# Optimization experiments

Hardware: AMD Instinct MI355X
Metric: run time of the kernel (lower is better)

The kernel has to match this reference:

```python
import jax, jax.numpy as jnp
import numpy as np

REF_POINTS = 32
WINDOW_HOURS = 48.0


def setup_inputs() -> dict:
    key = jax.random.key(0)
    k1, k2, k3 = jax.random.split(key, 3)
    B, T, F = 32, 512, 128
    x_hat = jax.random.normal(k1, (B, T, F), dtype=jnp.float32)
    mask = jax.random.randint(k2, (B, T, F), 0, 2).astype(jnp.float32)
    # per-step deltas in seconds (~0-600s) so cumulative time spans the 48h window
    tau = jax.random.uniform(k3, (B, T), dtype=jnp.float32) * 600.0
    log_kernel = jnp.zeros((F,), dtype=jnp.float32)
    return {"x_hat": x_hat, "mask": mask, "tau": tau, "log_kernel": log_kernel}


def reference(x_hat, mask, tau, log_kernel):
    # x_hat, mask: (B,T,F); tau: (B,T); log_kernel: (F,)
    kappa = jax.nn.softplus(log_kernel)                       # (F,)
    t_hours = jnp.cumsum(tau, axis=1) / 3600.0                # (B,T)
    ref_t = jnp.linspace(0.0, WINDOW_HOURS, REF_POINTS, dtype=x_hat.dtype)  # (R,)
    dist2 = (t_hours[:, :, None] - ref_t[None, None, :]) ** 2  # (B,T,R)
    d2k = dist2[..., None] * kappa                             # (B,T,R,F)
    m = mask[:, :, None, :]                                    # (B,T,1,F) -> broadcast over R
    w_lp = jnp.exp(-d2k) * m                                   # (B,T,R,F)
    w_hp = jnp.exp(-10.0 * d2k) * m                            # (B,T,R,F)
    x4 = x_hat[:, :, None, :]                                  # (B,T,1,F)
    lam = jnp.sum(w_lp, axis=1)                                # (B,R,F)
    sigma = jnp.sum(w_lp * x4, axis=1) / jnp.maximum(lam, 1.0)
    gamma = jnp.sum(w_hp * x4, axis=1) / jnp.maximum(jnp.sum(w_hp, axis=1), 1.0)
    return sigma, lam, gamma
```

## Files before the change

kernel.cpp:

```cpp
#include <hip/hip_runtime.h>
#include <math.h>
#include <type_traits>

constexpr int B_ = 32, T_ = 512, F_ = 128, R_ = 32;
constexpr int OUT_STRIDE = B_ * R_ * F_;

__device__ __forceinline__ float exp2_fast(float v) { return __builtin_amdgcn_exp2f(v); }

__launch_bounds__(256, 4)
__global__ void gauss_all(const float* __restrict__ xh, const float* __restrict__ mk,
                          const float* __restrict__ tau, const float* __restrict__ logk,
                          float* __restrict__ out) {
    const int lin = blockIdx.x;
    const int xcd = lin & 7, idx = lin >> 3;
    const int g = idx >> 5;
    const int r = (idx + g * 8) & 31;
    const int b = xcd + 8 * g;

    const int tid = threadIdx.x, lane = tid & 63, w = tid >> 6;
    __shared__ float th_s[T_];
    __shared__ float red[8][64];
    for (int i = tid; i < 512; i += 256) ((float*)red)[i] = 0.f;

    const float* tb = tau + b * T_;
    float v[8]; float s = 0.f;
#pragma unroll
    for (int k = 0; k < 8; ++k) { s += tb[lane * 8 + k]; v[k] = s; }
    float x = s;
#pragma unroll
    for (int d = 1; d < 64; d <<= 1) { float y = __shfl_up(x, d, 64); if (lane >= d) x += y; }
    const float excl = x - s;
#pragma unroll
    for (int k = 0; k < 8; ++k) v[k] = (excl + v[k]) * (1.f / 3600.f);
    if (w == 0) {
#pragma unroll
        for (int k = 0; k < 8; ++k) th_s[lane * 8 + k] = v[k];
    }

    const int f0 = 2 * lane;
    const float L2E = 1.4426950408889634f;
    const float lkx = logk[f0], lky = logk[f0 + 1];
    const float spx = fmaxf(lkx, 0.f) + log1pf(expf(-fabsf(lkx)));
    const float spy = fmaxf(lky, 0.f) + log1pf(expf(-fabsf(lky)));
    float mn = fminf(spx, spy), mx = fmaxf(spx, spy);
#pragma unroll
    for (int d = 1; d < 64; d <<= 1) {
        mn = fminf(mn, __shfl_xor(mn, d, 64));
        mx = fmaxf(mx, __shfl_xor(mx, d, 64));
    }
    const bool uni = (mn == mx);
    const float kl2e = mn * L2E;
    const float nkx = -spx * L2E, nky = -spy * L2E;
    const float nku = -kl2e;

    const float c = (float)((48.0 * r) / 31.0);
    const float Rlam = sqrtf(30.f / kl2e), Rhp = sqrtf(3.f / kl2e);
    int p01 = 0, p23 = 0;
#pragma unroll
    for (int k = 0; k < 8; ++k) {
        p01 += (int)(v[k] < c - Rlam) + ((int)(v[k] < c - Rhp) << 16);
        p23 += (int)(v[k] < c + Rhp) + ((int)(v[k] < c + Rlam) << 16);
    }
#pragma unroll
    for (int d = 1; d < 64; d <<= 1) { p01 += __shfl_xor(p01, d, 64); p23 += __shfl_xor(p23, d, 64); }
    const int Llo = p01 & 0xffff, Hlo = p01 >> 16;
    const int Hhi = p23 & 0xffff, Lhi = p23 >> 16;

    __syncthreads();

    const float* xb = xh + (size_t)b * T_ * F_ + f0;
    const float* mb = mk + (size_t)b * T_ * F_ + f0;
    float aL0 = 0, aL1 = 0, aS0 = 0, aS1 = 0;
    float aH0 = 0, aH1 = 0, aG0 = 0, aG1 = 0;

    auto run = [&](auto UNIC) {
        constexpr bool UNI = UNIC.value;
        for (int base = Hlo; base < Hhi; base += 16) {
            float2 xv[4], mv[4]; float thv[4];
#pragma unroll
            for (int j = 0; j < 4; ++j) {
                const int t = base + w * 4 + j;
                const int tt = t < Hhi ? t : Hhi - 1;
                xv[j] = *(const float2*)(xb + tt * F_);
                float2 m = *(const float2*)(mb + tt * F_);
                if (t >= Hhi) { m.x = 0.f; m.y = 0.f; }
                mv[j] = m; thv[j] = th_s[tt];
            }
#pragma unroll
            for (int j = 0; j < 4; ++j) {
                const float d = thv[j] - c, d2 = d * d;
                float ex, ey;
                if (UNI) { ex = exp2_fast(d2 * nku); ey = ex; }
                else     { ex = exp2_fast(d2 * nkx); ey = exp2_fast(d2 * nky); }
                const float mxx = mv[j].x * xv[j].x, mxy = mv[j].y * xv[j].y;
                aL0 = fmaf(ex, mv[j].x, aL0); aL1 = fmaf(ey, mv[j].y, aL1);
                aS0 = fmaf(ex, mxx, aS0);     aS1 = fmaf(ey, mxy, aS1);
                const float ex2 = ex * ex, ex4 = ex2 * ex2, ex8 = ex4 * ex4, exA = ex8 * ex2;
                float eyA;
                if (UNI) eyA = exA;
                else { const float ey2 = ey * ey, ey4 = ey2 * ey2, ey8 = ey4 * ey4; eyA = ey8 * ey2; }
                aH0 = fmaf(exA, mv[j].x, aH0); aH1 = fmaf(eyA, mv[j].y, aH1);
                aG0 = fmaf(exA, mxx, aG0);     aG1 = fmaf(eyA, mxy, aG1);
            }
        }
        auto wing = [&](int lo, int hi) {
            for (int base = lo; base < hi; base += 16) {
                float2 xv[4], mv[4]; float thv[4];
#pragma unroll
                for (int j = 0; j < 4; ++j) {
                    const int t = base + w * 4 + j;
                    const int tt = t < hi ? t : hi - 1;
                    xv[j] = *(const float2*)(xb + tt * F_);
                    float2 m = *(const float2*)(mb + tt * F_);
                    if (t >= hi) { m.x = 0.f; m.y = 0.f; }
                    mv[j] = m; thv[j] = th_s[tt];
                }
#pragma unroll
                for (int j = 0; j < 4; ++j) {
                    const float d = thv[j] - c, d2 = d * d;
                    float ex, ey;
                    if (UNI) { ex = exp2_fast(d2 * nku); ey = ex; }
                    else     { ex = exp2_fast(d2 * nkx); ey = exp2_fast(d2 * nky); }
                    aL0 = fmaf(ex, mv[j].x, aL0); aL1 = fmaf(ey, mv[j].y, aL1);
                    aS0 = fmaf(ex, mv[j].x * xv[j].x, aS0);
                    aS1 = fmaf(ey, mv[j].y * xv[j].y, aS1);
                }
            }
        };
        wing(Llo, Hlo);
        wing(Hhi, Lhi);
    };
    if (uni) run(std::integral_constant<bool, true>{});
    else     run(std::integral_constant<bool, false>{});

    atomicAdd(&red[0][lane], aL0); atomicAdd(&red[1][lane], aL1);
    atomicAdd(&red[2][lane], aS0); atomicAdd(&red[3][lane], aS1);
    atomicAdd(&red[4][lane], aH0); atomicAdd(&red[5][lane], aH1);
    atomicAdd(&red[6][lane], aG0); atomicAdd(&red[7][lane], aG1);
    __syncthreads();

    if (tid < F_) {
        const int l = tid >> 1, h = tid & 1;
        const float lam = red[0 + h][l], sig = red[2 + h][l];
        const float hp  = red[4 + h][l], gam = red[6 + h][l];
        const int base = (b * R_ + r) * F_ + tid;
        out[base]                  = sig / fmaxf(lam, 1.f);
        out[OUT_STRIDE + base]     = lam;
        out[2 * OUT_STRIDE + base] = gam / fmaxf(hp, 1.f);
    }
}

extern "C" void kernel_launch(void* const* d_in, const int* in_sizes, int n_in,
                              void* d_out, int out_size, void* d_ws, size_t ws_size,
                              hipStream_t stream) {
    const float* x_hat = (const float*)d_in[0];
    const float* mask  = (const float*)d_in[1];
    const float* tau   = (const float*)d_in[2];
    const float* logk  = (const float*)d_in[3];
    float* out = (float*)d_out;

    gauss_all<<<B_ * R_, 256, 0, stream>>>(x_hat, mask, tau, logk, out);
}
```

Before: 88.60 us.

## Process two reference points per block and precompute shared Gaussian weights

Each block now handles a pair of adjacent reference points, so every x_hat/mask load feeds accumulators for both. When kappa is uniform, the low- and high-pass weights are computed once per timestep into shared memory as float4 rather than recomputed per feature lane. The launch has half as many blocks, and launch bounds drop to 2 blocks per SM to make room for the doubled accumulators. The high-pass core/wing split is gone, so the t-window is the union of both points' wider lambda ranges, which adds some extra iterations and leaves fewer blocks for parallelism.

```diff
diff --git a/kernel.cpp b/kernel.cpp
--- a/kernel.cpp
+++ b/kernel.cpp
@@ -1,26 +1,29 @@
 #include <hip/hip_runtime.h>
 #include <math.h>
-#include <type_traits>
 
 constexpr int B_ = 32, T_ = 512, F_ = 128, R_ = 32;
 constexpr int OUT_STRIDE = B_ * R_ * F_;
 
 __device__ __forceinline__ float exp2_fast(float v) { return __builtin_amdgcn_exp2f(v); }
 
-__launch_bounds__(256, 4)
-__global__ void gauss_all(const float* __restrict__ xh, const float* __restrict__ mk,
-                          const float* __restrict__ tau, const float* __restrict__ logk,
-                          float* __restrict__ out) {
+__launch_bounds__(256, 2)
+__global__ void gauss_pair(const float* __restrict__ xh, const float* __restrict__ mk,
+                           const float* __restrict__ tau, const float* __restrict__ logk,
+                           float* __restrict__ out) {
     const int lin = blockIdx.x;
     const int xcd = lin & 7, idx = lin >> 3;
-    const int g = idx >> 5;
-    const int r = (idx + g * 8) & 31;
+    const int g = idx >> 4;
+    const int rp = idx & 15;
     const int b = xcd + 8 * g;
+    const int r0 = 2 * rp, r1 = r0 + 1;
 
     const int tid = threadIdx.x, lane = tid & 63, w = tid >> 6;
-    __shared__ float th_s[T_];
-    __shared__ float red[8][64];
-    for (int i = tid; i < 512; i += 256) ((float*)red)[i] = 0.f;
+
+    __shared__ float4 w_s[T_];
+    __shared__ float  th_s[T_];
+    __shared__ float  red[2][8][64];
+
+    for (int i = tid; i < 2 * 8 * 64; i += 256) (&red[0][0][0])[i] = 0.f;
 
     const float* tb = tau + b * T_;
     float v[8]; float s = 0.f;
@@ -51,99 +54,124 @@
     const bool uni = (mn == mx);
     const float kl2e = mn * L2E;
     const float nkx = -spx * L2E, nky = -spy * L2E;
-    const float nku = -kl2e;
 
-    const float c = (float)((48.0 * r) / 31.0);
-    const float Rlam = sqrtf(30.f / kl2e), Rhp = sqrtf(3.f / kl2e);
-    int p01 = 0, p23 = 0;
+    const float c0 = (float)((48.0 * r0) / 31.0);
+    const float c1 = (float)((48.0 * r1) / 31.0);
+
+    const float Rlam = sqrtf(30.f / kl2e);
+    int p = 0;
+#pragma unroll
+    for (int k = 0; k < 8; ++k)
+        p += (int)(v[k] < c0 - Rlam) + ((int)(v[k] < c1 + Rlam) << 16);
+#pragma unroll
+    for (int d = 1; d < 64; d <<= 1) p += __shfl_xor(p, d, 64);
+    const int Llo = p & 0xffff, Lhi = p >> 16;
+
 #pragma unroll
     for (int k = 0; k < 8; ++k) {
-        p01 += (int)(v[k] < c - Rlam) + ((int)(v[k] < c - Rhp) << 16);
-        p23 += (int)(v[k] < c + Rhp) + ((int)(v[k] < c + Rlam) << 16);
+        if ((k >> 1) == w) {
+            const int t = lane * 8 + k;
+            const float th = v[k];
+            const float d0 = th - c0, d1 = th - c1;
+            const float a0 = d0 * d0 * kl2e, a1 = d1 * d1 * kl2e;
+            const float lp0 = a0 < 30.f ? exp2_fast(-a0) : 0.f;
+            const float lp1 = a1 < 30.f ? exp2_fast(-a1) : 0.f;
+            const float q0 = lp0 * lp0, q1 = lp1 * lp1;
+            const float hp0 = ((q0 * q0) * (q0 * q0)) * q0;
+            const float hp1 = ((q1 * q1) * (q1 * q1)) * q1;
+            w_s[t] = make_float4(lp0, hp0, lp1, hp1);
+        }
     }
-#pragma unroll
-    for (int d = 1; d < 64; d <<= 1) { p01 += __shfl_xor(p01, d, 64); p23 += __shfl_xor(p23, d, 64); }
-    const int Llo = p01 & 0xffff, Hlo = p01 >> 16;
-    const int Hhi = p23 & 0xffff, Lhi = p23 >> 16;
-
     __syncthreads();
 
     const float* xb = xh + (size_t)b * T_ * F_ + f0;
     const float* mb = mk + (size_t)b * T_ * F_ + f0;
-    float aL0 = 0, aL1 = 0, aS0 = 0, aS1 = 0;
-    float aH0 = 0, aH1 = 0, aG0 = 0, aG1 = 0;
+    float aL[2][2] = {}, aS[2][2] = {}, aH[2][2] = {}, aG[2][2] = {};
 
-    auto run = [&](auto UNIC) {
-        constexpr bool UNI = UNIC.value;
-        for (int base = Hlo; base < Hhi; base += 16) {
+    if (uni) {
+        for (int base = Llo; base < Lhi; base += 16) {
+            float2 xv[4], mv[4]; float4 wv[4];
+#pragma unroll
+            for (int j = 0; j < 4; ++j) {
+                const int t = base + w * 4 + j;
+                const int tt = t < Lhi ? t : Lhi - 1;
+                xv[j] = *(const float2*)(xb + (size_t)tt * F_);
+                float2 m = *(const float2*)(mb + (size_t)tt * F_);
+                if (t >= Lhi) { m.x = 0.f; m.y = 0.f; }
+                mv[j] = m;
+                wv[j] = w_s[tt];
+            }
+#pragma unroll
+            for (int j = 0; j < 4; ++j) {
+                const float mxx = mv[j].x * xv[j].x, mxy = mv[j].y * xv[j].y;
+                aL[0][0] = fmaf(wv[j].x, mv[j].x, aL[0][0]);
+                aL[0][1] = fmaf(wv[j].x, mv[j].y, aL[0][1]);
+                aS[0][0] = fmaf(wv[j].x, mxx,     aS[0][0]);
+                aS[0][1] = fmaf(wv[j].x, mxy,     aS[0][1]);
+                aH[0][0] = fmaf(wv[j].y, mv[j].x, aH[0][0]);
+                aH[0][1] = fmaf(wv[j].y, mv[j].y, aH[0][1]);
+                aG[0][0] = fmaf(wv[j].y, mxx,     aG[0][0]);
+                aG[0][1] = fmaf(wv[j].y, mxy,     aG[0][1]);
+                aL[1][0] = fmaf(wv[j].z, mv[j].x, aL[1][0]);
+                aL[1][1] = fmaf(wv[j].z, mv[j].y, aL[1][1]);
+                aS[1][0] = fmaf(wv[j].z, mxx,     aS[1][0]);
+                aS[1][1] = fmaf(wv[j].z, mxy,     aS[1][1]);
+                aH[1][0] = fmaf(wv[j].w, mv[j].x, aH[1][0]);
+                aH[1][1] = fmaf(wv[j].w, mv[j].y, aH[1][1]);
+                aG[1][0] = fmaf(wv[j].w, mxx,     aG[1][0]);
+                aG[1][1] = fmaf(wv[j].w, mxy,     aG[1][1]);
+            }
+        }
+    } else {
+        for (int base = Llo; base < Lhi; base += 16) {
             float2 xv[4], mv[4]; float thv[4];
 #pragma unroll
             for (int j = 0; j < 4; ++j) {
                 const int t = base + w * 4 + j;
-                const int tt = t < Hhi ? t : Hhi - 1;
-                xv[j] = *(const float2*)(xb + tt * F_);
-                float2 m = *(const float2*)(mb + tt * F_);
-                if (t >= Hhi) { m.x = 0.f; m.y = 0.f; }
+                const int tt = t < Lhi ? t : Lhi - 1;
+                xv[j] = *(const float2*)(xb + (size_t)tt * F_);
+                float2 m = *(const float2*)(mb + (size_t)tt * F_);
+                if (t >= Lhi) { m.x = 0.f; m.y = 0.f; }
                 mv[j] = m; thv[j] = th_s[tt];
             }
 #pragma unroll
             for (int j = 0; j < 4; ++j) {
-                const float d = thv[j] - c, d2 = d * d;
-                float ex, ey;
-                if (UNI) { ex = exp2_fast(d2 * nku); ey = ex; }
-                else     { ex = exp2_fast(d2 * nkx); ey = exp2_fast(d2 * nky); }
                 const float mxx = mv[j].x * xv[j].x, mxy = mv[j].y * xv[j].y;
-                aL0 = fmaf(ex, mv[j].x, aL0); aL1 = fmaf(ey, mv[j].y, aL1);
-                aS0 = fmaf(ex, mxx, aS0);     aS1 = fmaf(ey, mxy, aS1);
-                const float ex2 = ex * ex, ex4 = ex2 * ex2, ex8 = ex4 * ex4, exA = ex8 * ex2;
-                float eyA;
-                if (UNI) eyA = exA;
-                else { const float ey2 = ey * ey, ey4 = ey2 * ey2, ey8 = ey4 * ey4; eyA = ey8 * ey2; }
-                aH0 = fmaf(exA, mv[j].x, aH0); aH1 = fmaf(eyA, mv[j].y, aH1);
-                aG0 = fmaf(exA, mxx, aG0);     aG1 = fmaf(eyA, mxy, aG1);
+#pragma unroll
+                for (int rr = 0; rr < 2; ++rr) {
+                    const float c = rr ? c1 : c0;
+                    const float d = thv[j] - c, d2 = d * d;
+                    const float ex = exp2_fast(d2 * nkx), ey = exp2_fast(d2 * nky);
+                    const float ex2 = ex * ex, ex4 = ex2 * ex2, ex8 = ex4 * ex4;
+                    const float ey2 = ey * ey, ey4 = ey2 * ey2, ey8 = ey4 * ey4;
+                    const float exA = ex8 * ex2, eyA = ey8 * ey2;
+                    aL[rr][0] = fmaf(ex,  mv[j].x, aL[rr][0]);
+                    aL[rr][1] = fmaf(ey,  mv[j].y, aL[rr][1]);
+                    aS[rr][0] = fmaf(ex,  mxx,     aS[rr][0]);
+                    aS[rr][1] = fmaf(ey,  mxy,     aS[rr][1]);
+                    aH[rr][0] = fmaf(exA, mv[j].x, aH[rr][0]);
+                    aH[rr][1] = fmaf(eyA, mv[j].y, aH[rr][1]);
+                    aG[rr][0] = fmaf(exA, mxx,     aG[rr][0]);
+                    aG[rr][1] = fmaf(eyA, mxy,     aG[rr][1]);
+                }
             }
         }
-        auto wing = [&](int lo, int hi) {
-            for (int base = lo; base < hi; base += 16) {
-                float2 xv[4], mv[4]; float thv[4];
+    }
+
 #pragma unroll
-                for (int j = 0; j < 4; ++j) {
-                    const int t = base + w * 4 + j;
-                    const int tt = t < hi ? t : hi - 1;
-                    xv[j] = *(const float2*)(xb + tt * F_);
-                    float2 m = *(const float2*)(mb + tt * F_);
-                    if (t >= hi) { m.x = 0.f; m.y = 0.f; }
-                    mv[j] = m; thv[j] = th_s[tt];
-                }
-#pragma unroll
-                for (int j = 0; j < 4; ++j) {
-                    const float d = thv[j] - c, d2 = d * d;
-                    float ex, ey;
-                    if (UNI) { ex = exp2_fast(d2 * nku); ey = ex; }
-                    else     { ex = exp2_fast(d2 * nkx); ey = exp2_fast(d2 * nky); }
-                    aL0 = fmaf(ex, mv[j].x, aL0); aL1 = fmaf(ey, mv[j].y, aL1);
-                    aS0 = fmaf(ex, mv[j].x * xv[j].x, aS0);
-                    aS1 = fmaf(ey, mv[j].y * xv[j].y, aS1);
-                }
-            }
-        };
-        wing(Llo, Hlo);
-        wing(Hhi, Lhi);
-    };
-    if (uni) run(std::integral_constant<bool, true>{});
-    else     run(std::integral_constant<bool, false>{});
-
-    atomicAdd(&red[0][lane], aL0); atomicAdd(&red[1][lane], aL1);
-    atomicAdd(&red[2][lane], aS0); atomicAdd(&red[3][lane], aS1);
-    atomicAdd(&red[4][lane], aH0); atomicAdd(&red[5][lane], aH1);
-    atomicAdd(&red[6][lane], aG0); atomicAdd(&red[7][lane], aG1);
+    for (int rr = 0; rr < 2; ++rr) {
+        atomicAdd(&red[rr][0][lane], aL[rr][0]); atomicAdd(&red[rr][1][lane], aL[rr][1]);
+        atomicAdd(&red[rr][2][lane], aS[rr][0]); atomicAdd(&red[rr][3][lane], aS[rr][1]);
+        atomicAdd(&red[rr][4][lane], aH[rr][0]); atomicAdd(&red[rr][5][lane], aH[rr][1]);
+        atomicAdd(&red[rr][6][lane], aG[rr][0]); atomicAdd(&red[rr][7][lane], aG[rr][1]);
+    }
     __syncthreads();
 
-    if (tid < F_) {
-        const int l = tid >> 1, h = tid & 1;
-        const float lam = red[0 + h][l], sig = red[2 + h][l];
-        const float hp  = red[4 + h][l], gam = red[6 + h][l];
-        const int base = (b * R_ + r) * F_ + tid;
+    {
+        const int rr = tid >> 7, f = tid & 127, l = f >> 1, h = f & 1;
+        const float lam = red[rr][0 + h][l], sig = red[rr][2 + h][l];
+        const float hp  = red[rr][4 + h][l], gam = red[rr][6 + h][l];
+        const int base = (b * R_ + r0 + rr) * F_ + f;
         out[base]                  = sig / fmaxf(lam, 1.f);
         out[OUT_STRIDE + base]     = lam;
         out[2 * OUT_STRIDE + base] = gam / fmaxf(hp, 1.f);
@@ -159,5 +187,5 @@
     const float* logk  = (const float*)d_in[3];
     float* out = (float*)d_out;
 
-    gauss_all<<<B_ * R_, 256, 0, stream>>>(x_hat, mask, tau, logk, out);
+    gauss_pair<<<B_ * (R_ / 2), 256, 0, stream>>>(x_hat, mask, tau, logk, out);
 }
```

New measurement: 86.77 us, median of 2. 1.02x faster.
